# Performance work log

Hardware: AMD Instinct MI355X
Metric: run time of the kernel (lower is better)

## Reference

```python
import jax, jax.numpy as jnp
import numpy as np

B, N, NT, ET = 8, 38, 9, 4
R, E = 416, 378  # repeat_num, edge steps (E = R - N)
H = D = 128      # nhid, nout
L = 12           # num_flow_layer
GCN_LAYERS = 3
SHIFT = 2.0      # sigmoid_shift


def setup_inputs() -> dict:
    key = jax.random.key(0)
    ks = jax.random.split(key, 16)
    inp = {}
    inp['x'] = jax.random.normal(ks[0], (B, N, NT), jnp.float32)
    inp['adj'] = jax.random.normal(ks[1], (B, ET, N, N), jnp.float32)
    inp['x_deq'] = jax.random.normal(ks[2], (B, N, NT), jnp.float32)
    inp['adj_deq'] = jax.random.normal(ks[3], (B, E, ET), jnp.float32)
    inp['mask_node'] = jax.random.randint(ks[4], (R, N), 0, 2).astype(bool)
    inp['mask_edge'] = jax.random.randint(ks[5], (R, N, N), 0, 2).astype(bool)
    inp['index_select_edge'] = jax.random.randint(ks[6], (E, 2), 0, N)
    inp['emb_w'] = jax.random.normal(ks[7], (NT, H), jnp.float32) * 0.1
    inp['gc_w'] = jax.random.normal(ks[8], (GCN_LAYERS, ET - 1, H, H), jnp.float32) * 0.05
    inp['gc_b'] = jnp.zeros((GCN_LAYERS, H), jnp.float32)
    inp['nw1'] = jax.random.normal(ks[9], (L, D, H), jnp.float32) * 0.05
    inp['nb1'] = jnp.zeros((L, H), jnp.float32)
    inp['nw2'] = jax.random.normal(ks[10], (L, H, 2 * NT), jnp.float32) * 0.05
    inp['nb2'] = jnp.zeros((L, 2 * NT), jnp.float32)
    inp['ew1'] = jax.random.normal(ks[11], (L, 3 * D, H), jnp.float32) * 0.05
    inp['eb1'] = jnp.zeros((L, H), jnp.float32)
    inp['ew2'] = jax.random.normal(ks[12], (L, H, 2 * ET), jnp.float32) * 0.05
    inp['eb2'] = jnp.zeros((L, 2 * ET), jnp.float32)
    return inp


def _get_embs(x, adj, mask_node, mask_edge, index_select_edge, emb_w, gc_w, gc_b):
    # mask + repeat: (B,R,N,NT) and (B,R,3,N,N), flattened to B*R graphs
    adj3 = adj[:, :ET - 1]
    xm = jnp.where(mask_node[None, :, :, None], x[:, None, :, :], 0.0)
    xm = xm.reshape(B * R, N, NT)
    am = jnp.where(mask_edge[None, :, None, :, :], adj3[:, None, :, :, :], 0.0)
    am = am.reshape(B * R, ET - 1, N, N)
    # relational GCN: emb then per-relation conv, summed over relations
    h = xm @ emb_w  # (BR, N, H)
    for l in range(GCN_LAYERS):
        sup = jnp.einsum('bni,eio->beno', h, gc_w[l])      # (BR, 3, N, H)
        out = jnp.einsum('benm,bemo->bno', am, sup) + gc_b[l]
        h = jax.nn.relu(out) if l < GCN_LAYERS - 1 else out
    node_emb = h.reshape(B, R, N, D)
    graph_emb = node_emb.sum(axis=2)                        # (B, R, D)
    g_node = graph_emb[:, :N].reshape(B * N, D)
    g_edge = graph_emb[:, N:]                               # (B, E, D)
    ne = node_emb[:, N:]                                    # (B, E, N, D)
    idx = jnp.broadcast_to(index_select_edge[None, :, :, None], (B, E, 2, D))
    pairs = jnp.take_along_axis(ne, idx, axis=2)            # (B, E, 2, D)
    g_ne = jnp.concatenate([pairs, g_edge[:, :, None, :]], axis=2)
    return g_node, g_ne.reshape(B * E, 3 * D)


def _st(inp, w1, b1, w2, b2, out_dim):
    st = jnp.tanh(inp @ w1 + b1) @ w2 + b2
    s = jax.nn.sigmoid(st[:, :out_dim] + SHIFT)
    t = st[:, out_dim:]
    return s, t


def reference(x, adj, x_deq, adj_deq, mask_node, mask_edge, index_select_edge,
              emb_w, gc_w, gc_b, nw1, nb1, nw2, nb2, ew1, eb1, ew2, eb2):
    g_node, g_edge = _get_embs(x, adj, mask_node, mask_edge, index_select_edge,
                               emb_w, gc_w, gc_b)
    xd = x_deq.reshape(-1, NT)
    ad = adj_deq.reshape(-1, ET)
    xlj = jnp.zeros_like(xd)
    alj = jnp.zeros_like(ad)
    for i in range(L):
        ns, nt = _st(g_node, nw1[i], nb1[i], nw2[i], nb2[i], NT)
        xd = xd * ns + nt
        xlj = xlj + jnp.log(jnp.abs(ns) + 1e-20)
        es, et = _st(g_edge, ew1[i], eb1[i], ew2[i], eb2[i], ET)
        ad = ad * es + et
        alj = alj + jnp.log(jnp.abs(es) + 1e-20)
    return (xd.reshape(B, -1), ad.reshape(B, -1),
            xlj.reshape(B, -1).sum(-1), alj.reshape(B, -1).sum(-1))
```

## Files before the change

### kernel.cpp

```cpp
#include <hip/hip_runtime.h>
#include <stdint.h>
#include <math.h>

#define Bc   8
#define Nn   38
#define NTc  9
#define ETc  4
#define Rr   416
#define Ee   378
#define Hh   128
#define Ll   12
#define GL   3

typedef __attribute__((ext_vector_type(8))) short s16x8;
typedef __attribute__((ext_vector_type(4))) short s16x4;
typedef __attribute__((ext_vector_type(4))) float f32x4;

static const size_t WS_MN    = 0;
static const size_t WS_ME    = 15872;
static const size_t WS_H0    = 616576;
static const size_t WS_ST    = 772224;
static const size_t WS_GWT   = 1165440;
static const size_t WS_NWT   = 1460352;
static const size_t WS_EWT   = 1853568;
static const size_t WS_GNB   = 3033216;
static const size_t WS_GEDGE = 3111040;
static const size_t WS_SN    = 5433472;
static const size_t WS_TN    = 5564800;
static const size_t WS_SE    = 5696128;
static const size_t WS_TE    = 6276736;
static const size_t WS_PART  = 6857344;

__device__ __forceinline__ unsigned short f2bf(float f) {
  unsigned u = __float_as_uint(f);
  u += 0x7FFFu + ((u >> 16) & 1u);
  return (unsigned short)(u >> 16);
}
__device__ __forceinline__ float bf2f(unsigned short h) {
  return __uint_as_float(((unsigned)h) << 16);
}

__device__ __forceinline__ uint8_t mval(const void* src, int i, int mode) {
  if (mode == 0) return ((const int*)src)[i] != 0;
  if (mode == 1) return ((const float*)src)[i] != 0.0f;
  return ((const uint8_t*)src)[i] != 0;
}

__global__ void prep_masks(const void* __restrict__ mn_src, const void* __restrict__ me_src,
                           uint8_t* __restrict__ mn_dst, uint8_t* __restrict__ me_dst)
{
  __shared__ int s01, sf;
  if (threadIdx.x == 0) { s01 = 1; sf = 1; }
  __syncthreads();
  const uint32_t* p = (const uint32_t*)me_src;
  bool a01 = true, af = true;
  for (int i = threadIdx.x; i < 256; i += blockDim.x) {
    uint32_t v = p[i];
    if (v > 1u) a01 = false;
    if (v != 0u && v != 0x3f800000u) af = false;
  }
  if (!a01) atomicAnd(&s01, 0);
  if (!af)  atomicAnd(&sf, 0);
  __syncthreads();
  const int mode = s01 ? 0 : (sf ? 1 : 2);

  const int n_node = Rr * Nn;
  const int n_edge = Rr * Nn * Nn;
  const int tot = n_node + n_edge;
  for (int i = blockIdx.x * blockDim.x + threadIdx.x; i < tot; i += gridDim.x * blockDim.x) {
    if (i < n_node) mn_dst[i] = mval(mn_src, i, mode);
    else            me_dst[i - n_node] = mval(me_src, i - n_node, mode);
  }
}

__global__ void prep_weights(const float* __restrict__ gw, const float* __restrict__ nw1,
                             const float* __restrict__ ew1,
                             unsigned short* __restrict__ gwt, unsigned short* __restrict__ nwt,
                             unsigned short* __restrict__ ewt)
{
  const int NG = 9 * 128 * 128;
  const int NNw = 12 * 128 * 128;
  const int NEw = 12 * 128 * 384;
  int idx = blockIdx.x * blockDim.x + threadIdx.x;
  if (idx < NG) {
    int k = idx & 127, col = (idx >> 7) & 127, le = idx >> 14;
    gwt[idx] = f2bf(gw[((size_t)le * 128 + k) * 128 + col]);
  } else if (idx < NG + NNw) {
    int j = idx - NG;
    int k = j & 127, col = (j >> 7) & 127, i = j >> 14;
    nwt[j] = f2bf(nw1[((size_t)i * 128 + k) * 128 + col]);
  } else if (idx < NG + NNw + NEw) {
    int j = idx - NG - NNw;
    int k = j % 384; int rem = j / 384;
    int col = rem & 127, i = rem >> 7;
    ewt[j] = f2bf(ew1[((size_t)i * 384 + k) * 128 + col]);
  }
}

__global__ void h0_kernel(const float* __restrict__ x, const float* __restrict__ emb_w,
                          float* __restrict__ h0)
{
  int idx = blockIdx.x * blockDim.x + threadIdx.x;
  if (idx >= Bc * Nn * Hh) return;
  int bn = idx >> 7, o = idx & 127;
  float acc = 0.0f;
  #pragma unroll
  for (int i = 0; i < NTc; ++i) acc += x[bn * NTc + i] * emb_w[i * Hh + o];
  h0[idx] = acc;
}

__global__ void s_kernel(const float* __restrict__ h0, const float* __restrict__ gw,
                         unsigned short* __restrict__ St)
{
  int idx = blockIdx.x * blockDim.x + threadIdx.x;
  if (idx >= Bc * GL * Hh * 64) return;
  int m = idx & 63;
  int col = (idx >> 6) & 127;
  int t = idx >> 13;
  int e = t % GL, b = t / GL;
  float acc = 0.0f;
  if (m < Nn)
    for (int k = 0; k < Hh; ++k)
      acc += h0[(b * Nn + m) * Hh + k] * gw[((size_t)e * Hh + k) * Hh + col];
  St[idx] = (m < Nn) ? f2bf(acc) : (unsigned short)0;
}

__global__ __launch_bounds__(256, 3)
void gcn_mfma_kernel(const float* __restrict__ adj, const uint8_t* __restrict__ mn,
                     const uint8_t* __restrict__ me, const unsigned short* __restrict__ St,
                     const unsigned short* __restrict__ gwt, const float* __restrict__ gb,
                     const int* __restrict__ isel,
                     unsigned short* __restrict__ gnb, unsigned short* __restrict__ gedge)
{
  __shared__ char smem[47744];
  unsigned short* h_lds  = (unsigned short*)smem;
  unsigned short* supT   = (unsigned short*)(smem + 12288);
  unsigned short* am_lds = (unsigned short*)(smem + 28672);
  float*          ge     = (float*)(smem + 47104);
  unsigned char*  mnu    = (unsigned char*)(smem + 47616);

  const int tid = threadIdx.x;
  const int b = blockIdx.x / Rr;
  const int r = blockIdx.x - b * Rr;
  const int lane = tid & 63;
  const int wv = tid >> 6;
  const int lo = lane & 15;
  const int q  = lane >> 4;
  const int swz = (lo & 7) << 3;
  const int ct0 = 2 * wv;

  for (int idx = tid; idx < GL * 48 * 64; idx += 256) {
    int e = idx / (48 * 64);
    int rem = idx - e * (48 * 64);
    int n = rem >> 6, m = rem & 63;
    float v = 0.0f;
    if (n < Nn && m < Nn && me[r * (Nn * Nn) + n * Nn + m])
      v = adj[((b * ETc + e) * Nn + n) * Nn + m];
    am_lds[e * 3072 + n * 64 + (m ^ ((n & 7) << 3))] = f2bf(v);
  }
  if (tid < 64) mnu[tid] = (tid < Nn) ? mn[r * Nn + tid] : 0;
  __syncthreads();

  f32x4 outacc[3][2];

  for (int l = 0; l < GL; ++l) {
    #pragma unroll
    for (int ci = 0; ci < 2; ++ci) {
      float bias = gb[l * Hh + 16 * (ct0 + ci) + lo];
      f32x4 bv = {bias, bias, bias, bias};
      outacc[0][ci] = bv; outacc[1][ci] = bv; outacc[2][ci] = bv;
    }

    for (int e = 0; e < GL; ++e) {
      if (l == 0) {
        __syncthreads();
        {
          int scol = tid >> 1, skh = (tid & 1) * 32;
          const unsigned short* ssrc = St + ((size_t)(b * GL + e) * 128 + scol) * 64 + skh;
          int sswz = (scol & 7) << 3;
          #pragma unroll
          for (int j = 0; j < 4; ++j) {
            s16x8 v = *(const s16x8*)(ssrc + 8 * j);
            #pragma unroll
            for (int i = 0; i < 8; ++i)
              if (!mnu[skh + 8 * j + i]) v[i] = 0;
            *(s16x8*)&supT[scol * 64 + ((skh + 8 * j) ^ sswz)] = v;
          }
        }
        __syncthreads();
      } else {
        f32x4 sa[3][2];
        #pragma unroll
        for (int rt = 0; rt < 3; ++rt)
          #pragma unroll
          for (int ci = 0; ci < 2; ++ci)
            sa[rt][ci] = (f32x4){0.f, 0.f, 0.f, 0.f};

        const unsigned short* wb = gwt + (size_t)(l * GL + e) * (Hh * Hh);
        #pragma unroll
        for (int ks = 0; ks < 4; ++ks) {
          int k0 = 8 * q + 32 * ks;
          s16x8 b0 = *(const s16x8*)(wb + (16 * ct0 + lo) * 128 + k0);
          s16x8 b1 = *(const s16x8*)(wb + (16 * ct0 + 16 + lo) * 128 + k0);
          #pragma unroll
          for (int rt = 0; rt < 3; ++rt) {
            int row = lo + 16 * rt;
            s16x8 a = *(const s16x8*)&h_lds[row * 128 + (k0 ^ swz)];
            sa[rt][0] = __builtin_amdgcn_mfma_f32_16x16x32_bf16(a, b0, sa[rt][0], 0, 0, 0);
            sa[rt][1] = __builtin_amdgcn_mfma_f32_16x16x32_bf16(a, b1, sa[rt][1], 0, 0, 0);
          }
        }
        __syncthreads();
        #pragma unroll
        for (int rt = 0; rt < 3; ++rt)
          #pragma unroll
          for (int ci = 0; ci < 2; ++ci) {
            int col = 16 * (ct0 + ci) + lo;
            s16x4 pk;
            #pragma unroll
            for (int j = 0; j < 4; ++j) pk[j] = (short)f2bf(sa[rt][ci][j]);
            int k0 = 16 * rt + 4 * q;
            *(s16x4*)&supT[col * 64 + (k0 ^ swz)] = pk;
          }
        __syncthreads();
      }

      #pragma unroll
      for (int ks = 0; ks < 2; ++ks) {
        int k0 = 8 * q + 32 * ks;
        s16x8 b0 = *(const s16x8*)&supT[(16 * ct0 + lo) * 64 + (k0 ^ swz)];
        s16x8 b1 = *(const s16x8*)&supT[(16 * ct0 + 16 + lo) * 64 + (k0 ^ swz)];
        #pragma unroll
        for (int rt = 0; rt < 3; ++rt) {
          int row = lo + 16 * rt;
          s16x8 a = *(const s16x8*)&am_lds[e * 3072 + row * 64 + (k0 ^ swz)];
          outacc[rt][0] = __builtin_amdgcn_mfma_f32_16x16x32_bf16(a, b0, outacc[rt][0], 0, 0, 0);
          outacc[rt][1] = __builtin_amdgcn_mfma_f32_16x16x32_bf16(a, b1, outacc[rt][1], 0, 0, 0);
        }
      }
    }

    #pragma unroll
    for (int rt = 0; rt < 3; ++rt)
      #pragma unroll
      for (int ci = 0; ci < 2; ++ci) {
        int col = 16 * (ct0 + ci) + lo;
        #pragma unroll
        for (int j = 0; j < 4; ++j) {
          int row = 16 * rt + 4 * q + j;
          float v = outacc[rt][ci][j];
          if (l < GL - 1) v = fmaxf(v, 0.0f);
          h_lds[row * 128 + (col ^ ((row & 7) << 3))] = f2bf(v);
        }
      }
    __syncthreads();
  }

  if (tid < 128) {
    float s = 0.0f;
    for (int n = 0; n < Nn; ++n)
      s += bf2f(h_lds[n * 128 + (tid ^ ((n & 7) << 3))]);
    ge[tid] = s;
  }
  __syncthreads();

  if (r < Nn) {
    if (tid < 128) gnb[(size_t)(b * Nn + r) * Hh + tid] = f2bf(ge[tid]);
  } else {
    int ei = r - Nn;
    int i0 = isel[2 * ei], i1 = isel[2 * ei + 1];
    unsigned short* dst = gedge + (size_t)(b * Ee + ei) * 384;
    if (tid < 128) {
      dst[tid]        = h_lds[i0 * 128 + (tid ^ ((i0 & 7) << 3))];
      dst[128 + tid]  = h_lds[i1 * 128 + (tid ^ ((i1 & 7) << 3))];
      dst[256 + tid]  = f2bf(ge[tid]);
    }
  }
}

template<int IN_W, int OUT_D, int ROWS>
__global__ __launch_bounds__(256)
void st_mfma_kernel(const unsigned short* __restrict__ A,
                    const unsigned short* __restrict__ wt,
                    const float* __restrict__ b1,
                    const float* __restrict__ w2,
                    const float* __restrict__ b2,
                    float* __restrict__ s_out, float* __restrict__ t_out)
{
  constexpr int MT = (ROWS + 31) / 32;
  constexpr int OD2 = 2 * OUT_D;
  __shared__ unsigned short hid[32 * 136];
  const int tid = threadIdx.x;
  const int i = blockIdx.x / MT;
  const int mt = blockIdx.x - i * MT;
  const int row0 = mt * 32;
  const int lane = tid & 63, wv = tid >> 6;
  const int lo = lane & 15, q = lane >> 4;

  f32x4 acc[2][2];
  #pragma unroll
  for (int rt = 0; rt < 2; ++rt)
    #pragma unroll
    for (int ci = 0; ci < 2; ++ci)
      acc[rt][ci] = (f32x4){0.f, 0.f, 0.f, 0.f};

  int ra = row0 + lo;       if (ra >= ROWS) ra = 0;
  int rb = row0 + 16 + lo;  if (rb >= ROWS) rb = 0;
  const unsigned short* Ap0 = A + (size_t)ra * IN_W;
  const unsigned short* Ap1 = A + (size_t)rb * IN_W;
  const unsigned short* Bp0 = wt + ((size_t)i * 128 + 32 * wv + lo) * IN_W;
  const unsigned short* Bp1 = wt + ((size_t)i * 128 + 32 * wv + 16 + lo) * IN_W;

  #pragma unroll
  for (int ks = 0; ks < IN_W / 32; ++ks) {
    int k0 = 8 * q + 32 * ks;
    s16x8 a0 = *(const s16x8*)(Ap0 + k0);
    s16x8 a1 = *(const s16x8*)(Ap1 + k0);
    s16x8 b0 = *(const s16x8*)(Bp0 + k0);
    s16x8 b1 = *(const s16x8*)(Bp1 + k0);
    acc[0][0] = __builtin_amdgcn_mfma_f32_16x16x32_bf16(a0, b0, acc[0][0], 0, 0, 0);
    acc[0][1] = __builtin_amdgcn_mfma_f32_16x16x32_bf16(a0, b1, acc[0][1], 0, 0, 0);
    acc[1][0] = __builtin_amdgcn_mfma_f32_16x16x32_bf16(a1, b0, acc[1][0], 0, 0, 0);
    acc[1][1] = __builtin_amdgcn_mfma_f32_16x16x32_bf16(a1, b1, acc[1][1], 0, 0, 0);
  }

  #pragma unroll
  for (int rt = 0; rt < 2; ++rt)
    #pragma unroll
    for (int ci = 0; ci < 2; ++ci) {
      int col = 32 * wv + 16 * ci + lo;
      float bb = b1[i * 128 + col];
      #pragma unroll
      for (int j = 0; j < 4; ++j) {
        int row = 16 * rt + 4 * q + j;
        hid[row * 136 + col] = f2bf(tanhf(acc[rt][ci][j] + bb));
      }
    }
  __syncthreads();

  for (int idx = tid; idx < 32 * OD2; idx += 256) {
    int lr = idx / OD2, c = idx - lr * OD2;
    int gr = row0 + lr;
    if (gr < ROWS) {
      float a = b2[i * OD2 + c];
      for (int k = 0; k < 128; ++k)
        a += bf2f(hid[lr * 136 + k]) * w2[((size_t)i * 128 + k) * OD2 + c];
      if (c < OUT_D) s_out[((size_t)i * ROWS + gr) * OUT_D + c] = 1.0f / (1.0f + expf(-(a + 2.0f)));
      else           t_out[((size_t)i * ROWS + gr) * OUT_D + (c - OUT_D)] = a;
    }
  }
}

__global__ __launch_bounds__(256)
void combine_part(const float* __restrict__ x_deq, const float* __restrict__ adj_deq,
                  const float* __restrict__ sn, const float* __restrict__ tn,
                  const float* __restrict__ se, const float* __restrict__ te,
                  float* __restrict__ out, float* __restrict__ partials)
{
  const int blk = blockIdx.x, tid = threadIdx.x;
  const int b = blk >> 3, ch = blk & 7;
  float ljx = 0.0f, lja = 0.0f;

  for (int j = ch * 256 + tid; j < Nn * NTc; j += 2048) {
    int n = j / NTc, c = j - n * NTc;
    int row = b * Nn + n;
    float v = x_deq[b * (Nn * NTc) + j];
    #pragma unroll
    for (int i = 0; i < Ll; ++i) {
      float s = sn[((size_t)i * (Bc * Nn) + row) * NTc + c];
      float t = tn[((size_t)i * (Bc * Nn) + row) * NTc + c];
      v = v * s + t;
      ljx += logf(fabsf(s) + 1e-20f);
    }
    out[b * (Nn * NTc) + j] = v;
  }

  for (int j = ch * 256 + tid; j < Ee * ETc; j += 2048) {
    int e = j / ETc, c = j - e * ETc;
    int row = b * Ee + e;
    float v = adj_deq[b * (Ee * ETc) + j];
    #pragma unroll
    for (int i = 0; i < Ll; ++i) {
      float s = se[((size_t)i * (Bc * Ee) + row) * ETc + c];
      float t = te[((size_t)i * (Bc * Ee) + row) * ETc + c];
      v = v * s + t;
      lja += logf(fabsf(s) + 1e-20f);
    }
    out[Bc * Nn * NTc + b * (Ee * ETc) + j] = v;
  }

  __shared__ float red[256];
  red[tid] = ljx; __syncthreads();
  for (int st = 128; st > 0; st >>= 1) { if (tid < st) red[tid] += red[tid + st]; __syncthreads(); }
  if (tid == 0) partials[blk] = red[0];
  __syncthreads();
  red[tid] = lja; __syncthreads();
  for (int st = 128; st > 0; st >>= 1) { if (tid < st) red[tid] += red[tid + st]; __syncthreads(); }
  if (tid == 0) partials[64 + blk] = red[0];
}

__global__ void combine_lj(const float* __restrict__ partials, float* __restrict__ out)
{
  int tid = threadIdx.x;
  if (tid < Bc) {
    float sx = 0.0f, sa = 0.0f;
    #pragma unroll
    for (int ch = 0; ch < 8; ++ch) {
      sx += partials[tid * 8 + ch];
      sa += partials[64 + tid * 8 + ch];
    }
    out[Bc * Nn * NTc + Bc * Ee * ETc + tid] = sx;
    out[Bc * Nn * NTc + Bc * Ee * ETc + Bc + tid] = sa;
  }
}

extern "C" void kernel_launch(void* const* d_in, const int* in_sizes, int n_in,
                              void* d_out, int out_size, void* d_ws, size_t ws_size,
                              hipStream_t stream)
{
  const float* x       = (const float*)d_in[0];
  const float* adj     = (const float*)d_in[1];
  const float* x_deq   = (const float*)d_in[2];
  const float* adj_deq = (const float*)d_in[3];
  const void*  mn_src  = d_in[4];
  const void*  me_src  = d_in[5];
  const int*   isel    = (const int*)d_in[6];
  const float* emb_w   = (const float*)d_in[7];
  const float* gw      = (const float*)d_in[8];
  const float* gb      = (const float*)d_in[9];
  const float* nw1     = (const float*)d_in[10];
  const float* nb1     = (const float*)d_in[11];
  const float* nw2     = (const float*)d_in[12];
  const float* nb2     = (const float*)d_in[13];
  const float* ew1     = (const float*)d_in[14];
  const float* eb1     = (const float*)d_in[15];
  const float* ew2     = (const float*)d_in[16];
  const float* eb2     = (const float*)d_in[17];

  char* ws = (char*)d_ws;
  uint8_t* mn            = (uint8_t*)(ws + WS_MN);
  uint8_t* me            = (uint8_t*)(ws + WS_ME);
  float* h0              = (float*)(ws + WS_H0);
  unsigned short* St     = (unsigned short*)(ws + WS_ST);
  unsigned short* gwt    = (unsigned short*)(ws + WS_GWT);
  unsigned short* nwt    = (unsigned short*)(ws + WS_NWT);
  unsigned short* ewt    = (unsigned short*)(ws + WS_EWT);
  unsigned short* gnb    = (unsigned short*)(ws + WS_GNB);
  unsigned short* gedge  = (unsigned short*)(ws + WS_GEDGE);
  float* sn              = (float*)(ws + WS_SN);
  float* tn              = (float*)(ws + WS_TN);
  float* se              = (float*)(ws + WS_SE);
  float* te              = (float*)(ws + WS_TE);
  float* partials        = (float*)(ws + WS_PART);

  const int NW_TOT = 9 * 128 * 128 + 12 * 128 * 128 + 12 * 128 * 384;

  prep_masks<<<256, 256, 0, stream>>>(mn_src, me_src, mn, me);
  prep_weights<<<(NW_TOT + 255) / 256, 256, 0, stream>>>(gw, nw1, ew1, gwt, nwt, ewt);
  h0_kernel<<<(Bc * Nn * Hh + 255) / 256, 256, 0, stream>>>(x, emb_w, h0);
  s_kernel<<<(Bc * GL * Hh * 64 + 255) / 256, 256, 0, stream>>>(h0, gw, St);
  gcn_mfma_kernel<<<Bc * Rr, 256, 0, stream>>>(adj, mn, me, St, gwt, gb, isel, gnb, gedge);
  st_mfma_kernel<128, NTc, Bc * Nn><<<Ll * ((Bc * Nn + 31) / 32), 256, 0, stream>>>(
      gnb, nwt, nb1, nw2, nb2, sn, tn);
  st_mfma_kernel<384, ETc, Bc * Ee><<<Ll * ((Bc * Ee + 31) / 32), 256, 0, stream>>>(
      gedge, ewt, eb1, ew2, eb2, se, te);
  combine_part<<<Bc * 8, 256, 0, stream>>>(x_deq, adj_deq, sn, tn, se, te, (float*)d_out, partials);
  combine_lj<<<1, 64, 0, stream>>>(partials, (float*)d_out);
}
```

Before: 337.8 us.

## Feed layer-0 GCN support from global registers and drop per-relation barriers

Layer 0 no longer stages the precomputed support St into LDS behind two barriers. Each wave now loads its B fragments straight from global memory and applies the node mask with a precomputed 32-bit AND mask. In layers 1 and 2 the block-wide barriers around supT writes are removed, because each wave writes and reads only its own supT columns. The padded k-range of supT is zeroed once up front, and one barrier is kept before overwriting h_lds, which other waves read. This cuts synchronisation and LDS round-trips, at the cost of more global loads and correctness resting on per-wave column ownership.

```diff
diff --git a/kernel.cpp b/kernel.cpp
--- a/kernel.cpp
+++ b/kernel.cpp
@@ -159,71 +159,109 @@
     am_lds[e * 3072 + n * 64 + (m ^ ((n & 7) << 3))] = f2bf(v);
   }
   if (tid < 64) mnu[tid] = (tid < Nn) ? mn[r * Nn + tid] : 0;
-  __syncthreads();
+
+  {
+    int zcol = tid >> 1, zhalf = tid & 1;
+    int zsw = (zcol & 7) << 3;
+    *(s16x8*)&supT[zcol * 64 + ((48 + 8 * zhalf) ^ zsw)] = (s16x8){0,0,0,0,0,0,0,0};
+  }
+  __syncthreads();
+
+  uint32_t mkm[2][4];
+  #pragma unroll
+  for (int ks = 0; ks < 2; ++ks)
+    #pragma unroll
+    for (int d = 0; d < 4; ++d) {
+      int k0 = 32 * ks + 8 * q + 2 * d;
+      mkm[ks][d] = (mnu[k0] ? 0x0000FFFFu : 0u) | (mnu[k0 + 1] ? 0xFFFF0000u : 0u);
+    }
+
+  float bias[GL][2];
+  #pragma unroll
+  for (int l = 0; l < GL; ++l)
+    #pragma unroll
+    for (int ci = 0; ci < 2; ++ci)
+      bias[l][ci] = gb[l * Hh + 16 * (ct0 + ci) + lo];
 
   f32x4 outacc[3][2];
 
-  for (int l = 0; l < GL; ++l) {
+  #pragma unroll
+  for (int ci = 0; ci < 2; ++ci) {
+    f32x4 bv = {bias[0][ci], bias[0][ci], bias[0][ci], bias[0][ci]};
+    outacc[0][ci] = bv; outacc[1][ci] = bv; outacc[2][ci] = bv;
+  }
+  #pragma unroll
+  for (int e = 0; e < GL; ++e) {
+    const unsigned short* Sb = St + (size_t)(b * GL + e) * 128 * 64;
+    #pragma unroll
+    for (int ks = 0; ks < 2; ++ks) {
+      union { s16x8 v; uint32_t u[4]; } B0, B1;
+      B0.v = *(const s16x8*)(Sb + (16 * ct0 + lo) * 64 + 32 * ks + 8 * q);
+      B1.v = *(const s16x8*)(Sb + (16 * ct0 + 16 + lo) * 64 + 32 * ks + 8 * q);
+      #pragma unroll
+      for (int d = 0; d < 4; ++d) { B0.u[d] &= mkm[ks][d]; B1.u[d] &= mkm[ks][d]; }
+      #pragma unroll
+      for (int rt = 0; rt < 3; ++rt) {
+        s16x8 a = *(const s16x8*)&am_lds[e * 3072 + (lo + 16 * rt) * 64 + ((8 * q + 32 * ks) ^ swz)];
+        outacc[rt][0] = __builtin_amdgcn_mfma_f32_16x16x32_bf16(a, B0.v, outacc[rt][0], 0, 0, 0);
+        outacc[rt][1] = __builtin_amdgcn_mfma_f32_16x16x32_bf16(a, B1.v, outacc[rt][1], 0, 0, 0);
+      }
+    }
+  }
+  #pragma unroll
+  for (int rt = 0; rt < 3; ++rt)
     #pragma unroll
     for (int ci = 0; ci < 2; ++ci) {
-      float bias = gb[l * Hh + 16 * (ct0 + ci) + lo];
-      f32x4 bv = {bias, bias, bias, bias};
+      int col = 16 * (ct0 + ci) + lo;
+      #pragma unroll
+      for (int j = 0; j < 4; ++j) {
+        int row = 16 * rt + 4 * q + j;
+        h_lds[row * 128 + (col ^ ((row & 7) << 3))] = f2bf(fmaxf(outacc[rt][ci][j], 0.0f));
+      }
+    }
+  __syncthreads();
+
+  #pragma unroll
+  for (int l = 1; l < GL; ++l) {
+    #pragma unroll
+    for (int ci = 0; ci < 2; ++ci) {
+      f32x4 bv = {bias[l][ci], bias[l][ci], bias[l][ci], bias[l][ci]};
       outacc[0][ci] = bv; outacc[1][ci] = bv; outacc[2][ci] = bv;
     }
 
     for (int e = 0; e < GL; ++e) {
-      if (l == 0) {
-        __syncthreads();
-        {
-          int scol = tid >> 1, skh = (tid & 1) * 32;
-          const unsigned short* ssrc = St + ((size_t)(b * GL + e) * 128 + scol) * 64 + skh;
-          int sswz = (scol & 7) << 3;
+      f32x4 sa[3][2];
+      #pragma unroll
+      for (int rt = 0; rt < 3; ++rt)
+        #pragma unroll
+        for (int ci = 0; ci < 2; ++ci)
+          sa[rt][ci] = (f32x4){0.f, 0.f, 0.f, 0.f};
+
+      const unsigned short* wb = gwt + (size_t)(l * GL + e) * (Hh * Hh);
+      #pragma unroll
+      for (int ks = 0; ks < 4; ++ks) {
+        int k0 = 8 * q + 32 * ks;
+        s16x8 b0 = *(const s16x8*)(wb + (16 * ct0 + lo) * 128 + k0);
+        s16x8 b1 = *(const s16x8*)(wb + (16 * ct0 + 16 + lo) * 128 + k0);
+        #pragma unroll
+        for (int rt = 0; rt < 3; ++rt) {
+          s16x8 a = *(const s16x8*)&h_lds[(lo + 16 * rt) * 128 + (k0 ^ swz)];
+          sa[rt][0] = __builtin_amdgcn_mfma_f32_16x16x32_bf16(a, b0, sa[rt][0], 0, 0, 0);
+          sa[rt][1] = __builtin_amdgcn_mfma_f32_16x16x32_bf16(a, b1, sa[rt][1], 0, 0, 0);
+        }
+      }
+
+      #pragma unroll
+      for (int rt = 0; rt < 3; ++rt)
+        #pragma unroll
+        for (int ci = 0; ci < 2; ++ci) {
+          int col = 16 * (ct0 + ci) + lo;
+          s16x4 pk;
           #pragma unroll
-          for (int j = 0; j < 4; ++j) {
-            s16x8 v = *(const s16x8*)(ssrc + 8 * j);
-            #pragma unroll
-            for (int i = 0; i < 8; ++i)
-              if (!mnu[skh + 8 * j + i]) v[i] = 0;
-            *(s16x8*)&supT[scol * 64 + ((skh + 8 * j) ^ sswz)] = v;
-          }
+          for (int j = 0; j < 4; ++j) pk[j] = (short)f2bf(sa[rt][ci][j]);
+          int k0 = 16 * rt + 4 * q;
+          *(s16x4*)&supT[col * 64 + (k0 ^ swz)] = pk;
         }
-        __syncthreads();
-      } else {
-        f32x4 sa[3][2];
-        #pragma unroll
-        for (int rt = 0; rt < 3; ++rt)
-          #pragma unroll
-          for (int ci = 0; ci < 2; ++ci)
-            sa[rt][ci] = (f32x4){0.f, 0.f, 0.f, 0.f};
-
-        const unsigned short* wb = gwt + (size_t)(l * GL + e) * (Hh * Hh);
-        #pragma unroll
-        for (int ks = 0; ks < 4; ++ks) {
-          int k0 = 8 * q + 32 * ks;
-          s16x8 b0 = *(const s16x8*)(wb + (16 * ct0 + lo) * 128 + k0);
-          s16x8 b1 = *(const s16x8*)(wb + (16 * ct0 + 16 + lo) * 128 + k0);
-          #pragma unroll
-          for (int rt = 0; rt < 3; ++rt) {
-            int row = lo + 16 * rt;
-            s16x8 a = *(const s16x8*)&h_lds[row * 128 + (k0 ^ swz)];
-            sa[rt][0] = __builtin_amdgcn_mfma_f32_16x16x32_bf16(a, b0, sa[rt][0], 0, 0, 0);
-            sa[rt][1] = __builtin_amdgcn_mfma_f32_16x16x32_bf16(a, b1, sa[rt][1], 0, 0, 0);
-          }
-        }
-        __syncthreads();
-        #pragma unroll
-        for (int rt = 0; rt < 3; ++rt)
-          #pragma unroll
-          for (int ci = 0; ci < 2; ++ci) {
-            int col = 16 * (ct0 + ci) + lo;
-            s16x4 pk;
-            #pragma unroll
-            for (int j = 0; j < 4; ++j) pk[j] = (short)f2bf(sa[rt][ci][j]);
-            int k0 = 16 * rt + 4 * q;
-            *(s16x4*)&supT[col * 64 + (k0 ^ swz)] = pk;
-          }
-        __syncthreads();
-      }
 
       #pragma unroll
       for (int ks = 0; ks < 2; ++ks) {
@@ -232,14 +270,14 @@
         s16x8 b1 = *(const s16x8*)&supT[(16 * ct0 + 16 + lo) * 64 + (k0 ^ swz)];
         #pragma unroll
         for (int rt = 0; rt < 3; ++rt) {
-          int row = lo + 16 * rt;
-          s16x8 a = *(const s16x8*)&am_lds[e * 3072 + row * 64 + (k0 ^ swz)];
+          s16x8 a = *(const s16x8*)&am_lds[e * 3072 + (lo + 16 * rt) * 64 + (k0 ^ swz)];
           outacc[rt][0] = __builtin_amdgcn_mfma_f32_16x16x32_bf16(a, b0, outacc[rt][0], 0, 0, 0);
           outacc[rt][1] = __builtin_amdgcn_mfma_f32_16x16x32_bf16(a, b1, outacc[rt][1], 0, 0, 0);
         }
       }
     }
 
+    __syncthreads();
     #pragma unroll
     for (int rt = 0; rt < 3; ++rt)
       #pragma unroll
```

After: 330.5 us. 1.02x faster.
